# Optimization experiments

Hardware: AMD Instinct MI355X
Metric: run time of the kernel (lower is better)

Reference implementation:

```python
import jax, jax.numpy as jnp
import numpy as np

DIM = 512
HEAD_DIM = 32
HEADS = DIM // HEAD_DIM
WS = 7              # window_size
DISP = WS // 2      # cyclic shift displacement
SHIFTED = True


def _rel_indices(ws):
    # torch indexes pos_embedding with raw (possibly negative) distances;
    # negative python indices wrap modulo the dim size (2*ws-1).
    idx = np.array([[x, y] for x in range(ws) for y in range(ws)])
    d = idx[None, :, :] - idx[:, None, :]          # (ws^2, ws^2, 2)
    return np.mod(d, 2 * ws - 1)


def _mask(ws, disp, upper_lower, left_right):
    m = np.zeros((ws, ws, ws, ws), np.float32)
    if upper_lower:
        m[:-disp, :, -disp:, :] = -np.inf
        m[-disp:, :, :-disp, :] = -np.inf
    if left_right:
        m[:, -disp:, :, :-disp] = -np.inf
        m[:, :-disp, :, -disp:] = -np.inf
    return m.reshape(ws * ws, ws * ws)


def setup_inputs() -> dict:
    key = jax.random.key(0)
    ks = jax.random.split(key, 5)
    B, H, W = 32, 56, 56
    x = jax.random.normal(ks[0], (B, H, W, DIM), jnp.float32)
    w_qkv = jax.random.normal(ks[1], (DIM, 3 * DIM), jnp.float32) * 0.02
    pos_emb = jax.random.normal(ks[2], (2 * WS - 1, 2 * WS - 1, HEADS), jnp.float32)
    w_out = jax.random.normal(ks[3], (DIM, DIM), jnp.float32) * 0.02
    b_out = jax.random.normal(ks[4], (DIM,), jnp.float32) * 0.02
    return {"x": x, "w_qkv": w_qkv, "pos_emb": pos_emb, "w_out": w_out, "b_out": b_out}


def reference(x, w_qkv, pos_emb, w_out, b_out):
    rel = _rel_indices(WS)                         # static int constants
    ul_mask = jnp.asarray(_mask(WS, DISP, True, False))
    lr_mask = jnp.asarray(_mask(WS, DISP, False, True))

    B, H, W, _ = x.shape
    nw_h, nw_w = H // WS, W // WS

    if SHIFTED:
        x = jnp.roll(x, (-DISP, -DISP), axis=(1, 2))

    qkv = x @ w_qkv                                # (B,H,W,3*dim)

    def to_windows(t):
        # (B,H,W,dim) -> (B, heads, nw_h*nw_w, ws*ws, head_dim)
        t = t.reshape(B, nw_h, WS, nw_w, WS, HEADS, HEAD_DIM)
        return t.transpose(0, 5, 1, 3, 2, 4, 6).reshape(B, HEADS, nw_h * nw_w, WS * WS, HEAD_DIM)

    q, k, v = (to_windows(t) for t in jnp.split(qkv, 3, axis=-1))

    dots = jnp.einsum('bhwid,bhwjd->bhwij', q, k) * (HEAD_DIM ** -0.5)
    bias = pos_emb[rel[:, :, 0], rel[:, :, 1], :]  # (ws^2, ws^2, heads)
    dots = dots + bias.transpose(2, 0, 1)[None, :, None]

    if SHIFTED:
        dots = dots.at[:, :, -nw_w:].add(ul_mask)
        dots = dots.at[:, :, nw_w - 1::nw_w].add(lr_mask)

    attn = jax.nn.softmax(dots, axis=-1)
    out = jnp.einsum('bhwij,bhwjd->bhwid', attn, v)

    # (B,heads,nw,ws^2,d) -> (B,H,W,dim)
    out = out.reshape(B, HEADS, nw_h, nw_w, WS, WS, HEAD_DIM)
    out = out.transpose(0, 2, 4, 3, 5, 1, 6).reshape(B, H, W, DIM)
    out = out @ w_out + b_out

    if SHIFTED:
        out = jnp.roll(out, (DISP, DISP), axis=(1, 2))
    return out
```

## Files before the change

### kernel.cpp

```cpp
#include <hip/hip_runtime.h>
#include <hip/hip_bf16.h>
#include <stdint.h>


#define NWIN 64
#define NTOK 49
#define WIN_ELEMS 1568
#define HEAD_STRIDE 100352
#define BATCH_STRIDE 1605632
#define QKV_ELEMS 51380224
#define NTOKENS 100352
#define SCALE 0.17677669529663687f

typedef __attribute__((ext_vector_type(8))) short bf16x8;
typedef __attribute__((ext_vector_type(4))) float f32x4;

#define AS1 __attribute__((address_space(1)))
#define AS3 __attribute__((address_space(3)))

struct __align__(16) bf8 { __hip_bfloat16 h[8]; };

__device__ __forceinline__ void gload_lds16(const void* g, void* l) {
  __builtin_amdgcn_global_load_lds((const AS1 unsigned int*)g,
                                   (AS3 unsigned int*)l, 16, 0, 0);
}

__device__ __forceinline__ void token_decode(int t, int& b, int& i, int& j) {
  b = t / 3136;
  int r = t - b * 3136;
  i = r / 56;
  j = r - i * 56;
}

__global__ __launch_bounds__(256) void k_prep_lut(int* __restrict__ lutw,
                                                  int* __restrict__ luto) {
  int t = blockIdx.x * 256 + threadIdx.x;
  int b, i, j;
  token_decode(t, b, i, j);
  int win = (i / 7) * 8 + (j / 7);
  int pos = (i % 7) * 7 + (j % 7);
  lutw[t] = b * BATCH_STRIDE + win * WIN_ELEMS + pos * 32;
  int di = i + 3; if (di >= 56) di -= 56;
  int dj = j + 3; if (dj >= 56) dj -= 56;
  luto[t] = ((b * 56 + di) * 56 + dj) * 512;
}

__global__ __launch_bounds__(256) void k_prep_x(const float* __restrict__ x,
                                                __hip_bfloat16* __restrict__ xb) {
  int idx = blockIdx.x * 256 + threadIdx.x;
  int t = idx >> 6;
  int g = idx & 63;
  int b, i, j;
  token_decode(t, b, i, j);
  int si = i + 3; if (si >= 56) si -= 56;
  int sj = j + 3; if (sj >= 56) sj -= 56;
  const float* src = x + ((size_t)(b * 56 + si) * 56 + sj) * 512 + g * 8;
  float4 a0 = *(const float4*)src;
  float4 a1 = *(const float4*)(src + 4);
  bf8 o;
  o.h[0] = __float2bfloat16(a0.x); o.h[1] = __float2bfloat16(a0.y);
  o.h[2] = __float2bfloat16(a0.z); o.h[3] = __float2bfloat16(a0.w);
  o.h[4] = __float2bfloat16(a1.x); o.h[5] = __float2bfloat16(a1.y);
  o.h[6] = __float2bfloat16(a1.z); o.h[7] = __float2bfloat16(a1.w);
  int slot = ((g * 8) ^ ((t & 7) << 3));
  *(bf8*)(xb + (size_t)t * 512 + slot) = o;
}

__global__ __launch_bounds__(256) void k_transpose(const float* __restrict__ in,
                                                   __hip_bfloat16* __restrict__ out,
                                                   int K, int N) {
  __shared__ float tl[64][65];
  const int nb = blockIdx.x * 64, kb = blockIdx.y * 64;
  const int tid = threadIdx.x;
#pragma unroll
  for (int s = 0; s < 16; ++s) {
    int idx = s * 256 + tid; int r = idx >> 6, c = idx & 63;
    tl[r][c] = in[(size_t)(kb + r) * N + nb + c];
  }
  __syncthreads();
#pragma unroll
  for (int s = 0; s < 16; ++s) {
    int idx = s * 256 + tid; int r = idx >> 6, c = idx & 63;
    int row = nb + r;
    int col = (kb + c) ^ ((row & 7) << 3);
    out[(size_t)row * K + col] = __float2bfloat16(tl[c][r]);
  }
}

__global__ __launch_bounds__(256) void k_prep_bias(const float* __restrict__ pe,
                                                   float* __restrict__ biasT) {
  int id = blockIdx.x * 256 + threadIdx.x;
  int whid = id >> 12;
  int wtype = whid >> 4, h = whid & 15;
  int mid = id & 4095;
  int mf = mid >> 10, r = (mid >> 8) & 3, lane = (mid >> 2) & 63, nf = mid & 3;
  int key = mf * 16 + (lane >> 4) * 4 + r;
  int query = nf * 16 + (lane & 15);
  float v;
  if (key >= 49 || query >= 49) {
    v = -1e30f;
  } else {
    int i = query, j = key;
    int xi = i / 7, yi = i - xi * 7;
    int xj = j / 7, yj = j - xj * 7;
    int dx = xj - xi; if (dx < 0) dx += 13;
    int dy = yj - yi; if (dy < 0) dy += 13;
    v = pe[(dx * 13 + dy) * 16 + h];
    if ((wtype & 1) && ((xi >= 4) != (xj >= 4))) v = -1e30f;
    if ((wtype & 2) && ((yi >= 4) != (yj >= 4))) v = -1e30f;
  }
  biasT[id] = v;
}

__global__ __launch_bounds__(256) void k_qkv_mfma(
    const __hip_bfloat16* __restrict__ xb, const __hip_bfloat16* __restrict__ wbt,
    const int* __restrict__ lutw,
    __hip_bfloat16* __restrict__ qb, __hip_bfloat16* __restrict__ kb,
    __hip_bfloat16* __restrict__ vb) {
  __shared__ __align__(16) short As[2][128 * 64];
  __shared__ __align__(16) short Bs[2][128 * 64];
  const int tid = threadIdx.x;
  const int lid = blockIdx.x;
  const int wid = (lid & 7) * 1176 + (lid >> 3);
  const int t0 = (wid / 12) * 128;
  const int n0 = (wid % 12) * 128;
  const int lane = tid & 63, wave = tid >> 6;
  const int wm = wave >> 1, wn = wave & 1;

  const __hip_bfloat16* asrc[4];
  const __hip_bfloat16* bsrc[4];
#pragma unroll
  for (int s = 0; s < 4; ++s) {
    int c = s * 256 + tid;
    int row = c >> 3, kc = c & 7;
    asrc[s] = xb + (size_t)(t0 + row) * 512 + kc * 8;
    bsrc[s] = wbt + (size_t)(n0 + row) * 512 + kc * 8;
  }

  f32x4 acc[4][4] = {};
  const int arow = wm * 64 + (lane & 15);
  const int brow = wn * 64 + (lane & 15);
  const int koff = (lane >> 4) * 8;
  const int sw = (lane & 7) << 3;

#pragma unroll
  for (int s = 0; s < 4; ++s) {
    gload_lds16(asrc[s], (char*)As[0] + wave * 1024 + s * 4096);
    gload_lds16(bsrc[s], (char*)Bs[0] + wave * 1024 + s * 4096);
  }

  for (int t = 0; t < 8; ++t) {
    const int buf = t & 1;
    if (t < 7) {
      const int kt = (t + 1) * 64;
#pragma unroll
      for (int s = 0; s < 4; ++s) {
        gload_lds16(asrc[s] + kt, (char*)As[buf ^ 1] + wave * 1024 + s * 4096);
        gload_lds16(bsrc[s] + kt, (char*)Bs[buf ^ 1] + wave * 1024 + s * 4096);
      }
      asm volatile("s_waitcnt vmcnt(8)" ::: "memory");
    } else {
      asm volatile("s_waitcnt vmcnt(0)" ::: "memory");
    }
    __builtin_amdgcn_s_barrier();
    __builtin_amdgcn_sched_barrier(0);

    bf16x8 af[2][4], bfr[2][4];
#pragma unroll
    for (int kk = 0; kk < 2; ++kk) {
      const int eo = (kk * 32 + koff) ^ sw;
#pragma unroll
      for (int mf = 0; mf < 4; ++mf)
        af[kk][mf] = *(const bf16x8*)&As[buf][(arow + mf * 16) * 64 + eo];
#pragma unroll
      for (int nf = 0; nf < 4; ++nf)
        bfr[kk][nf] = *(const bf16x8*)&Bs[buf][(brow + nf * 16) * 64 + eo];
    }
    __builtin_amdgcn_s_setprio(1);
#pragma unroll
    for (int kk = 0; kk < 2; ++kk)
#pragma unroll
      for (int mf = 0; mf < 4; ++mf)
#pragma unroll
        for (int nf = 0; nf < 4; ++nf)
          acc[mf][nf] = __builtin_amdgcn_mfma_f32_16x16x32_bf16(
              af[kk][mf], bfr[kk][nf], acc[mf][nf], 0, 0, 0);
    __builtin_amdgcn_s_setprio(0);
    __builtin_amdgcn_s_barrier();
    __builtin_amdgcn_sched_barrier(0);
  }

  __hip_bfloat16* obs[4];
#pragma unroll
  for (int nf = 0; nf < 4; ++nf) {
    int n = n0 + wn * 64 + nf * 16 + (lane & 15);
    int sp = n >> 9, hc = n & 511, h = hc >> 5, d = hc & 31;
    obs[nf] = (sp == 0 ? qb : (sp == 1 ? kb : vb)) + (size_t)h * HEAD_STRIDE + d;
  }
  const int tbase = t0 + wm * 64 + (lane >> 4) * 4;
  int woff[4][4];
#pragma unroll
  for (int mf = 0; mf < 4; ++mf)
#pragma unroll
    for (int r = 0; r < 4; ++r)
      woff[mf][r] = lutw[tbase + mf * 16 + r];
#pragma unroll
  for (int mf = 0; mf < 4; ++mf)
#pragma unroll
    for (int r = 0; r < 4; ++r) {
      size_t off = (size_t)woff[mf][r];
#pragma unroll
      for (int nf = 0; nf < 4; ++nf)
        obs[nf][off] = __float2bfloat16(acc[mf][nf][r]);
    }
}

__global__ __launch_bounds__(256) void k_attn_mfma(
    const __hip_bfloat16* __restrict__ qb, const __hip_bfloat16* __restrict__ kb,
    const __hip_bfloat16* __restrict__ vb, const float* __restrict__ biasT,
    __hip_bfloat16* __restrict__ ab) {
  __shared__ __align__(16) __hip_bfloat16 P[4][64 * 72];
  __shared__ __align__(16) __hip_bfloat16 VT[4][32 * 64];
  const int tid = threadIdx.x, lane = tid & 63, wave = tid >> 6;
  const int gid = blockIdx.x * 4 + wave;
  const int win = gid & 63, h = (gid >> 6) & 15;
  const int wtype = (((win >> 3) == 7) ? 1 : 0) | (((win & 7) == 7) ? 2 : 0);
  const size_t qkbase = (size_t)gid * WIN_ELEMS;
  const int fr = lane & 15, fo = (lane >> 4) * 8;

  bf8 v8[4];
#pragma unroll
  for (int it = 0; it < 4; ++it) {
    int c = it * 64 + lane;
    if (c < 196) v8[it] = *(const bf8*)(vb + qkbase + (size_t)c * 8);
  }

  bf16x8 kf[4], qf[4];
#pragma unroll
  for (int f = 0; f < 4; ++f) {
    kf[f] = *(const bf16x8*)(kb + qkbase + (size_t)(f * 16 + fr) * 32 + fo);
    qf[f] = *(const bf16x8*)(qb + qkbase + (size_t)(f * 16 + fr) * 32 + fo);
  }

  __hip_bfloat16* vtw = VT[wave];
  {
    bf16x8 zz = {};
#pragma unroll
    for (int z = 0; z < 4; ++z) *(bf16x8*)&vtw[z * 512 + lane * 8] = zz;
  }
#pragma unroll
  for (int it = 0; it < 4; ++it) {
    int c = it * 64 + lane;
    if (c < 196) {
      int pos = c >> 2, d0 = (c & 3) * 8;
#pragma unroll
      for (int u = 0; u < 8; ++u) {
        int d = d0 + u;
        vtw[d * 64 + (pos ^ ((d & 7) << 3))] = v8[it].h[u];
      }
    }
  }

  f32x4 sacc[4][4] = {};
#pragma unroll
  for (int mf = 0; mf < 4; ++mf)
#pragma unroll
    for (int nf = 0; nf < 4; ++nf)
      sacc[mf][nf] = __builtin_amdgcn_mfma_f32_16x16x32_bf16(
          kf[mf], qf[nf], sacc[mf][nf], 0, 0, 0);

  const float* bp = biasT + (size_t)(wtype * 16 + h) * 4096;
#pragma unroll
  for (int mf = 0; mf < 4; ++mf)
#pragma unroll
    for (int r = 0; r < 4; ++r) {
      float4 bv = *(const float4*)(bp + ((mf * 4 + r) * 64 + lane) * 4);
      sacc[mf][0][r] = fmaf(sacc[mf][0][r], SCALE, bv.x);
      sacc[mf][1][r] = fmaf(sacc[mf][1][r], SCALE, bv.y);
      sacc[mf][2][r] = fmaf(sacc[mf][2][r], SCALE, bv.z);
      sacc[mf][3][r] = fmaf(sacc[mf][3][r], SCALE, bv.w);
    }

  float inv[4];
#pragma unroll
  for (int nf = 0; nf < 4; ++nf) {
    float m = sacc[0][nf][0];
#pragma unroll
    for (int mf = 0; mf < 4; ++mf)
#pragma unroll
      for (int r = 0; r < 4; ++r) m = fmaxf(m, sacc[mf][nf][r]);
    m = fmaxf(m, __shfl_xor(m, 16));
    m = fmaxf(m, __shfl_xor(m, 32));
    float sum = 0.f;
#pragma unroll
    for (int mf = 0; mf < 4; ++mf)
#pragma unroll
      for (int r = 0; r < 4; ++r) {
        float e = __expf(sacc[mf][nf][r] - m);
        sacc[mf][nf][r] = e;
        sum += e;
      }
    sum += __shfl_xor(sum, 16);
    sum += __shfl_xor(sum, 32);
    inv[nf] = 1.0f / sum;
  }

  __hip_bfloat16* pw = P[wave];
#pragma unroll
  for (int mf = 0; mf < 4; ++mf)
#pragma unroll
    for (int r = 0; r < 4; ++r) {
      int key = mf * 16 + (lane >> 4) * 4 + r;
#pragma unroll
      for (int nf = 0; nf < 4; ++nf) {
        int query = nf * 16 + fr;
        pw[query * 72 + key] = __float2bfloat16(sacc[mf][nf][r] * inv[nf]);
      }
    }

  f32x4 oacc[4][2] = {};
#pragma unroll
  for (int kk = 0; kk < 2; ++kk) {
    bf16x8 vf[2];
#pragma unroll
    for (int n2 = 0; n2 < 2; ++n2) {
      int d = n2 * 16 + fr;
      vf[n2] = *(const bf16x8*)&vtw[d * 64 + ((kk * 32 + fo) ^ ((d & 7) << 3))];
    }
#pragma unroll
    for (int mf = 0; mf < 4; ++mf) {
      bf16x8 pa = *(const bf16x8*)&pw[(mf * 16 + fr) * 72 + kk * 32 + fo];
#pragma unroll
      for (int n2 = 0; n2 < 2; ++n2)
        oacc[mf][n2] = __builtin_amdgcn_mfma_f32_16x16x32_bf16(
            pa, vf[n2], oacc[mf][n2], 0, 0, 0);
    }
  }

#pragma unroll
  for (int mf = 0; mf < 4; ++mf)
#pragma unroll
    for (int r = 0; r < 4; ++r) {
      int row = mf * 16 + (lane >> 4) * 4 + r;
      if (row < 49) {
#pragma unroll
        for (int n2 = 0; n2 < 2; ++n2)
          ab[qkbase + (size_t)row * 32 + n2 * 16 + fr] =
              __float2bfloat16(oacc[mf][n2][r]);
      }
    }
}

__global__ __launch_bounds__(256) void k_out_mfma(
    const __hip_bfloat16* __restrict__ ab, const __hip_bfloat16* __restrict__ wot,
    const int* __restrict__ lutw, const int* __restrict__ luto,
    const float* __restrict__ bias, float* __restrict__ out) {
  __shared__ __align__(16) short As[2][128 * 64];
  __shared__ __align__(16) short Bs[2][128 * 64];
  const int tid = threadIdx.x;
  const int lid = blockIdx.x;
  const int wid = (lid & 7) * 392 + (lid >> 3);
  const int t0 = (wid >> 2) * 128;
  const int n0 = (wid & 3) * 128;
  const int lane = tid & 63, wave = tid >> 6;
  const int wm = wave >> 1, wn = wave & 1;

  size_t aoff[4];
  const __hip_bfloat16* bsrc[4];
#pragma unroll
  for (int s = 0; s < 4; ++s) {
    int c = s * 256 + tid;
    int row = c >> 3, kc = c & 7;
    aoff[s] = (size_t)lutw[t0 + row] + (size_t)(kc >> 2) * HEAD_STRIDE + (kc & 3) * 8;
    bsrc[s] = wot + (size_t)(n0 + row) * 512 + kc * 8;
  }

  f32x4 acc[4][4] = {};
  const int arow = wm * 64 + (lane & 15);
  const int brow = wn * 64 + (lane & 15);
  const int koff = (lane >> 4) * 8;
  const int sw = (lane & 7) << 3;

#pragma unroll
  for (int s = 0; s < 4; ++s) {
    gload_lds16(ab + aoff[s], (char*)As[0] + wave * 1024 + s * 4096);
    gload_lds16(bsrc[s], (char*)Bs[0] + wave * 1024 + s * 4096);
  }

  for (int t = 0; t < 8; ++t) {
    const int buf = t & 1;
    if (t < 7) {
      const int kt = (t + 1) * 64;
      size_t hoff = (size_t)(kt >> 5) * HEAD_STRIDE;
#pragma unroll
      for (int s = 0; s < 4; ++s) {
        gload_lds16(ab + aoff[s] + hoff, (char*)As[buf ^ 1] + wave * 1024 + s * 4096);
        gload_lds16(bsrc[s] + kt, (char*)Bs[buf ^ 1] + wave * 1024 + s * 4096);
      }
      asm volatile("s_waitcnt vmcnt(8)" ::: "memory");
    } else {
      asm volatile("s_waitcnt vmcnt(0)" ::: "memory");
    }
    __builtin_amdgcn_s_barrier();
    __builtin_amdgcn_sched_barrier(0);

    bf16x8 af[2][4], bfr[2][4];
#pragma unroll
    for (int kk = 0; kk < 2; ++kk) {
      const int eo = kk * 32 + koff;
#pragma unroll
      for (int mf = 0; mf < 4; ++mf)
        af[kk][mf] = *(const bf16x8*)&As[buf][(arow + mf * 16) * 64 + eo];
#pragma unroll
      for (int nf = 0; nf < 4; ++nf)
        bfr[kk][nf] = *(const bf16x8*)&Bs[buf][(brow + nf * 16) * 64 + (eo ^ sw)];
    }
    __builtin_amdgcn_s_setprio(1);
#pragma unroll
    for (int kk = 0; kk < 2; ++kk)
#pragma unroll
      for (int mf = 0; mf < 4; ++mf)
#pragma unroll
        for (int nf = 0; nf < 4; ++nf)
          acc[mf][nf] = __builtin_amdgcn_mfma_f32_16x16x32_bf16(
              af[kk][mf], bfr[kk][nf], acc[mf][nf], 0, 0, 0);
    __builtin_amdgcn_s_setprio(0);
    __builtin_amdgcn_s_barrier();
    __builtin_amdgcn_sched_barrier(0);
  }

  float bia[4];
#pragma unroll
  for (int nf = 0; nf < 4; ++nf)
    bia[nf] = bias[n0 + wn * 64 + nf * 16 + (lane & 15)];

  const int tbase = t0 + wm * 64 + (lane >> 4) * 4;
  int ooff[4][4];
#pragma unroll
  for (int mf = 0; mf < 4; ++mf)
#pragma unroll
    for (int r = 0; r < 4; ++r)
      ooff[mf][r] = luto[tbase + mf * 16 + r];
#pragma unroll
  for (int mf = 0; mf < 4; ++mf) {
#pragma unroll
    for (int r = 0; r < 4; ++r) {
      float* op = out + (size_t)ooff[mf][r] + n0 + wn * 64 + (lane & 15);
#pragma unroll
      for (int nf = 0; nf < 4; ++nf) op[nf * 16] = acc[mf][nf][r] + bia[nf];
    }
  }
}

extern "C" void kernel_launch(void* const* d_in, const int* in_sizes, int n_in,
                              void* d_out, int out_size, void* d_ws, size_t ws_size,
                              hipStream_t stream) {
  const float* x     = (const float*)d_in[0];
  const float* w_qkv = (const float*)d_in[1];
  const float* pe    = (const float*)d_in[2];
  const float* w_out = (const float*)d_in[3];
  const float* b_out = (const float*)d_in[4];
  float* out = (float*)d_out;

  __hip_bfloat16* qb  = (__hip_bfloat16*)d_ws;
  __hip_bfloat16* kb  = qb + (size_t)QKV_ELEMS;
  __hip_bfloat16* vb  = kb + (size_t)QKV_ELEMS;
  __hip_bfloat16* xb  = vb + (size_t)QKV_ELEMS;
  __hip_bfloat16* ab  = xb;
  __hip_bfloat16* wbt = xb + (size_t)QKV_ELEMS;
  __hip_bfloat16* wot = wbt + (size_t)(1536 * 512);
  float* biasT = (float*)(wot + (size_t)(512 * 512));
  int* lutw = (int*)(biasT + 262144);
  int* luto = lutw + NTOKENS;

  k_prep_lut<<<dim3(392), dim3(256), 0, stream>>>(lutw, luto);
  k_prep_x<<<dim3(25088), dim3(256), 0, stream>>>(x, xb);
  k_transpose<<<dim3(24, 8), dim3(256), 0, stream>>>(w_qkv, wbt, 512, 1536);
  k_transpose<<<dim3(8, 8), dim3(256), 0, stream>>>(w_out, wot, 512, 512);
  k_prep_bias<<<dim3(1024), dim3(256), 0, stream>>>(pe, biasT);
  k_qkv_mfma<<<dim3(9408), dim3(256), 0, stream>>>(xb, wbt, lutw, qb, kb, vb);
  k_attn_mfma<<<dim3(8192), dim3(256), 0, stream>>>(qb, kb, vb, biasT, ab);
  k_out_mfma<<<dim3(3136), dim3(256), 0, stream>>>(ab, wot, lutw, luto, b_out, out);
}
```

Measured before the change: 542.4 us.

## Load V MFMA fragments directly from global, pack P stores, raise MFMA priority

```diff
diff --git a/kernel.cpp b/kernel.cpp
--- a/kernel.cpp
+++ b/kernel.cpp
@@ -30,6 +30,12 @@
   int r = t - b * 3136;
   i = r / 56;
   j = r - i * 56;
+}
+
+__device__ __forceinline__ unsigned pack_bf2(float a, float b) {
+  __hip_bfloat16 x = __float2bfloat16(a), y = __float2bfloat16(b);
+  unsigned short ux = *(unsigned short*)&x, uy = *(unsigned short*)&y;
+  return (unsigned)ux | ((unsigned)uy << 16);
 }
 
 __global__ __launch_bounds__(256) void k_prep_lut(int* __restrict__ lutw,
@@ -220,7 +226,6 @@
     const __hip_bfloat16* __restrict__ vb, const float* __restrict__ biasT,
     __hip_bfloat16* __restrict__ ab) {
   __shared__ __align__(16) __hip_bfloat16 P[4][64 * 72];
-  __shared__ __align__(16) __hip_bfloat16 VT[4][32 * 64];
   const int tid = threadIdx.x, lane = tid & 63, wave = tid >> 6;
   const int gid = blockIdx.x * 4 + wave;
   const int win = gid & 63, h = (gid >> 6) & 15;
@@ -228,12 +233,16 @@
   const size_t qkbase = (size_t)gid * WIN_ELEMS;
   const int fr = lane & 15, fo = (lane >> 4) * 8;
 
-  bf8 v8[4];
-#pragma unroll
-  for (int it = 0; it < 4; ++it) {
-    int c = it * 64 + lane;
-    if (c < 196) v8[it] = *(const bf8*)(vb + qkbase + (size_t)c * 8);
-  }
+  bf16x8 vfr[2][2];
+  const short* vbs = (const short*)(vb + qkbase);
+#pragma unroll
+  for (int kk = 0; kk < 2; ++kk)
+#pragma unroll
+    for (int n2 = 0; n2 < 2; ++n2) {
+      const short* vp = vbs + (kk * 32 + fo) * 32 + n2 * 16 + fr;
+#pragma unroll
+      for (int j = 0; j < 8; ++j) vfr[kk][n2][j] = vp[j * 32];
+    }
 
   bf16x8 kf[4], qf[4];
 #pragma unroll
@@ -242,32 +251,15 @@
     qf[f] = *(const bf16x8*)(qb + qkbase + (size_t)(f * 16 + fr) * 32 + fo);
   }
 
-  __hip_bfloat16* vtw = VT[wave];
-  {
-    bf16x8 zz = {};
-#pragma unroll
-    for (int z = 0; z < 4; ++z) *(bf16x8*)&vtw[z * 512 + lane * 8] = zz;
-  }
-#pragma unroll
-  for (int it = 0; it < 4; ++it) {
-    int c = it * 64 + lane;
-    if (c < 196) {
-      int pos = c >> 2, d0 = (c & 3) * 8;
-#pragma unroll
-      for (int u = 0; u < 8; ++u) {
-        int d = d0 + u;
-        vtw[d * 64 + (pos ^ ((d & 7) << 3))] = v8[it].h[u];
-      }
-    }
-  }
-
   f32x4 sacc[4][4] = {};
+  __builtin_amdgcn_s_setprio(1);
 #pragma unroll
   for (int mf = 0; mf < 4; ++mf)
 #pragma unroll
     for (int nf = 0; nf < 4; ++nf)
       sacc[mf][nf] = __builtin_amdgcn_mfma_f32_16x16x32_bf16(
           kf[mf], qf[nf], sacc[mf][nf], 0, 0, 0);
+  __builtin_amdgcn_s_setprio(0);
 
   const float* bp = biasT + (size_t)(wtype * 16 + h) * 4096;
 #pragma unroll
@@ -309,32 +301,29 @@
 #pragma unroll
   for (int mf = 0; mf < 4; ++mf)
 #pragma unroll
-    for (int r = 0; r < 4; ++r) {
+    for (int r = 0; r < 4; r += 2) {
       int key = mf * 16 + (lane >> 4) * 4 + r;
 #pragma unroll
       for (int nf = 0; nf < 4; ++nf) {
         int query = nf * 16 + fr;
-        pw[query * 72 + key] = __float2bfloat16(sacc[mf][nf][r] * inv[nf]);
+        *(unsigned*)&pw[query * 72 + key] =
+            pack_bf2(sacc[mf][nf][r] * inv[nf], sacc[mf][nf][r + 1] * inv[nf]);
       }
     }
 
   f32x4 oacc[4][2] = {};
 #pragma unroll
   for (int kk = 0; kk < 2; ++kk) {
-    bf16x8 vf[2];
-#pragma unroll
-    for (int n2 = 0; n2 < 2; ++n2) {
-      int d = n2 * 16 + fr;
-      vf[n2] = *(const bf16x8*)&vtw[d * 64 + ((kk * 32 + fo) ^ ((d & 7) << 3))];
-    }
+    __builtin_amdgcn_s_setprio(1);
 #pragma unroll
     for (int mf = 0; mf < 4; ++mf) {
       bf16x8 pa = *(const bf16x8*)&pw[(mf * 16 + fr) * 72 + kk * 32 + fo];
 #pragma unroll
       for (int n2 = 0; n2 < 2; ++n2)
         oacc[mf][n2] = __builtin_amdgcn_mfma_f32_16x16x32_bf16(
-            pa, vf[n2], oacc[mf][n2], 0, 0, 0);
-    }
+            pa, vfr[kk][n2], oacc[mf][n2], 0, 0, 0);
+    }
+    __builtin_amdgcn_s_setprio(0);
   }
 
 #pragma unroll
```

Measured after the change: 538.4 us. No clear change (-0.7%).
